# Performance work log

Measured on AMD Instinct MI355X. Metric: run time of the kernel, lower is better.

The kernel has to match this reference:

```python
import jax, jax.numpy as jnp
import numpy as np
import math

N_HEAD = 16
ROPE_BASE = 10000.0


def _rope_as_in_source(x):
    """Faithful replication of RotaryPositionalEmbeddings.forward applied to
    x of shape [B, H, T, hd] (called after transpose in the source, so
    seq_len = x.size(1) = H: angles are indexed by head index, not position)."""
    B, H, T, hd = x.shape
    theta = 1.0 / (ROPE_BASE ** (jnp.arange(0, hd, 2, dtype=jnp.float32) / hd))  # [hd/2]
    ang = jnp.arange(H, dtype=jnp.float32)[:, None] * theta[None, :]  # [H, hd/2]
    cos = jnp.cos(ang)[None, :, None, :]  # [1, H, 1, hd/2]
    sin = jnp.sin(ang)[None, :, None, :]
    xr = x.reshape(B, H, T, hd // 2, 2)
    out = jnp.stack([
        xr[..., 0] * cos - xr[..., 1] * sin,
        xr[..., 1] * cos + xr[..., 0] * sin,
    ], axis=-1)
    return out.reshape(B, H, T, hd)


def setup_inputs() -> dict:
    key = jax.random.key(0)
    ks = jax.random.split(key, 5)
    B, T, C = 2, 2048, 1024
    s = 0.02
    return {
        "x": jax.random.normal(ks[0], (B, T, C), dtype=jnp.float32),
        "W_attn": jax.random.normal(ks[1], (C, 3 * C), dtype=jnp.float32) * s,
        "b_attn": jnp.zeros((3 * C,), dtype=jnp.float32),
        "W_proj": jax.random.normal(ks[2], (C, C), dtype=jnp.float32) * s,
        "b_proj": jnp.zeros((C,), dtype=jnp.float32),
    }


def reference(x, W_attn, b_attn, W_proj, b_proj):
    B, T, C = x.shape
    H = N_HEAD
    hd = C // H
    qkv = x @ W_attn + b_attn  # [B, T, 3C]
    q, k, v = jnp.split(qkv, 3, axis=2)
    # [B, T, H, hd] -> [B, H, T, hd]
    q = q.reshape(B, T, H, hd).transpose(0, 2, 1, 3)
    k = k.reshape(B, T, H, hd).transpose(0, 2, 1, 3)
    v = v.reshape(B, T, H, hd).transpose(0, 2, 1, 3)
    q = _rope_as_in_source(q)
    k = _rope_as_in_source(k)
    att = jnp.einsum("bhqd,bhkd->bhqk", q, k) * (1.0 / math.sqrt(hd))
    causal = jnp.tril(jnp.ones((T, T), dtype=bool))
    att = jnp.where(causal[None, None, :, :], att, -jnp.inf)
    att = jax.nn.softmax(att, axis=-1)
    y = jnp.einsum("bhqk,bhkd->bhqd", att, v)  # [B, H, T, hd]
    y = y.transpose(0, 2, 1, 3).reshape(B, T, C)
    return y @ W_proj + b_proj
```

## Files before the change

### kernel.cpp

```cpp
#include <hip/hip_runtime.h>

typedef __attribute__((ext_vector_type(8))) short bf16x8;
typedef __attribute__((ext_vector_type(4))) float f32x4;
typedef __attribute__((ext_vector_type(4))) unsigned int uint4v;
typedef unsigned short ushort_t;

#define BB 2
#define TT 2048
#define CC 1024
#define HH 16
#define HD 64
#define MM (BB * TT)
#define N3C (3 * CC)
#define KD 1024
#define NT64 16

__device__ __forceinline__ ushort_t f2b(float f) {
  unsigned u = __builtin_bit_cast(unsigned, f);
  u += 0x7fffu + ((u >> 16) & 1u);
  return (ushort_t)(u >> 16);
}

__device__ __forceinline__ unsigned pack2rne(float a, float b) {
  return (unsigned)f2b(a) | ((unsigned)f2b(b) << 16);
}

__device__ __forceinline__ unsigned pack2bf(float a, float b) {
  unsigned ua = (__builtin_bit_cast(unsigned, a) + 0x8000u) >> 16;
  unsigned ub = (__builtin_bit_cast(unsigned, b) + 0x8000u) & 0xffff0000u;
  return ua | ub;
}

__device__ __forceinline__ float fexp2(float x) {
#if __has_builtin(__builtin_amdgcn_exp2f)
  return __builtin_amdgcn_exp2f(x);
#else
  return __expf(x * 0.6931471805599453f);
#endif
}

__device__ __forceinline__ f32x4 mfma16(bf16x8 a, bf16x8 b, f32x4 c) {
  return __builtin_amdgcn_mfma_f32_16x16x32_bf16(a, b, c, 0, 0, 0);
}

__device__ __forceinline__ void load_lds16(const void* g, void* l) {
  __builtin_amdgcn_global_load_lds((const __attribute__((address_space(1))) void*)g,
                                   (__attribute__((address_space(3))) void*)l, 16, 0, 0);
}

#define BAR()   __builtin_amdgcn_s_barrier()
#define SB0()   __builtin_amdgcn_sched_barrier(0)
#define LGKM0() asm volatile("s_waitcnt lgkmcnt(0)" ::: "memory")

__global__ __launch_bounds__(256) void prep(const float* __restrict__ x,
                                            const float* __restrict__ Wa,
                                            const float* __restrict__ Wp,
                                            ushort_t* __restrict__ xb,
                                            ushort_t* __restrict__ wat,
                                            ushort_t* __restrict__ wpt) {
  const int blk = blockIdx.x, tid = threadIdx.x;
  if (blk < 4096) {
    int i = blk * 256 + tid;
    const float4 v = ((const float4*)x)[i];
    typedef __attribute__((ext_vector_type(4))) ushort_t us4;
    us4 r;
    r.x = f2b(v.x); r.y = f2b(v.y); r.z = f2b(v.z); r.w = f2b(v.w);
    ((us4*)xb)[i] = r;
    return;
  }
  __shared__ ushort_t tile[32][33];
  const float* W; ushort_t* Wt; int R, Nc, n0, r0;
  if (blk < 7168) {
    int tb = blk - 4096;
    W = Wa; Wt = wat; R = CC; Nc = N3C;
    n0 = (tb % 96) * 32; r0 = (tb / 96) * 32;
  } else {
    int tb = blk - 7168;
    W = Wp; Wt = wpt; R = CC; Nc = CC;
    n0 = (tb & 31) * 32; r0 = (tb >> 5) * 32;
  }
  const int c = tid & 31, rr = tid >> 5;
#pragma unroll
  for (int i = 0; i < 4; ++i) {
    int r = rr + i * 8;
    tile[r][c] = f2b(W[(size_t)(r0 + r) * Nc + n0 + c]);
  }
  __syncthreads();
#pragma unroll
  for (int i = 0; i < 4; ++i) {
    int r = rr + i * 8;
    Wt[(size_t)(n0 + r) * R + r0 + c] = tile[c][r];
  }
}

__global__ __launch_bounds__(512, 2) void qkv256(const ushort_t* __restrict__ A,
                                                 const ushort_t* __restrict__ Bt,
                                                 const float* __restrict__ bias,
                                                 ushort_t* __restrict__ qo,
                                                 ushort_t* __restrict__ ko,
                                                 ushort_t* __restrict__ vto) {
  extern __shared__ ushort_t lds[];
  ushort_t* As = lds;
  ushort_t* Bs = lds + 32768;

  const int tid = threadIdx.x, lane = tid & 63, wave = tid >> 6;
  const int l15 = lane & 15, quad = lane >> 4;
  const int wm = (wave >> 2) * 128, wn = (wave & 3) * 64;
  const int m0 = blockIdx.y * 256, n0 = blockIdx.x * 256;

  const int rw0 = tid >> 2, gc0 = (tid & 3) ^ (rw0 & 3);
  const ushort_t* sA0 = A + (size_t)(m0 + rw0) * KD + gc0 * 8;
  const ushort_t* sA1 = sA0 + (size_t)128 * KD;
  const ushort_t* sB0 = Bt + (size_t)(n0 + rw0) * KD + gc0 * 8;
  const ushort_t* sB1 = sB0 + (size_t)128 * KD;
  ushort_t* dA0 = As + tid * 8;
  ushort_t* dA1 = dA0 + 4096;
  ushort_t* dB0 = Bs + tid * 8;
  ushort_t* dB1 = dB0 + 4096;

  auto stA = [&](int tau, int kh) {
    const int so = ((tau & 1) * 2 + kh) * 8192;
    const int ko2 = tau * 64 + kh * 32;
    load_lds16(sA0 + ko2, dA0 + so);
    load_lds16(sA1 + ko2, dA1 + so);
  };
  auto stB = [&](int tau, int kh) {
    const int so = ((tau & 1) * 2 + kh) * 8192;
    const int ko2 = tau * 64 + kh * 32;
    load_lds16(sB0 + ko2, dB0 + so);
    load_lds16(sB1 + ko2, dB1 + so);
  };

  const int swc = (quad ^ (l15 & 3)) * 8;
  const int rdA = (wm + l15) * 32 + swc;
  const int rdB = (wn + l15) * 32 + swc;

  f32x4 acc[8][4] = {};

  stB(0, 0); stA(0, 0); stB(0, 1); stA(0, 1);
  stB(1, 0); stA(1, 0); stB(1, 1);
  asm volatile("s_waitcnt vmcnt(6)" ::: "memory");
  BAR();
  SB0();

  bf16x8 a[4], b0[4], b1[4];
  for (int t = 0; t < NT64; ++t) {
    const int par = t & 1;
    const ushort_t* aK0 = As + par * 16384;
    const ushort_t* aK1 = aK0 + 8192;
    const ushort_t* bK0 = Bs + par * 16384;
    const ushort_t* bK1 = bK0 + 8192;

#pragma unroll
    for (int j = 0; j < 4; ++j) b0[j] = *(const bf16x8*)&bK0[rdB + j * 512];
#pragma unroll
    for (int i = 0; i < 4; ++i) a[i] = *(const bf16x8*)&aK0[rdA + i * 512];
    if (t + 1 < NT64) stA(t + 1, 1);
    BAR();
    LGKM0();
    __builtin_amdgcn_s_setprio(1);
#pragma unroll
    for (int i = 0; i < 4; ++i)
#pragma unroll
      for (int j = 0; j < 4; ++j) acc[i][j] = mfma16(a[i], b0[j], acc[i][j]);
    __builtin_amdgcn_s_setprio(0);
    BAR();
    SB0();

#pragma unroll
    for (int i = 0; i < 4; ++i) a[i] = *(const bf16x8*)&aK0[rdA + (4 + i) * 512];
    if (t + 2 < NT64) stB(t + 2, 0);
    BAR();
    LGKM0();
    __builtin_amdgcn_s_setprio(1);
#pragma unroll
    for (int i = 0; i < 4; ++i)
#pragma unroll
      for (int j = 0; j < 4; ++j) acc[4 + i][j] = mfma16(a[i], b0[j], acc[4 + i][j]);
    __builtin_amdgcn_s_setprio(0);
    BAR();
    SB0();

#pragma unroll
    for (int j = 0; j < 4; ++j) b1[j] = *(const bf16x8*)&bK1[rdB + j * 512];
#pragma unroll
    for (int i = 0; i < 4; ++i) a[i] = *(const bf16x8*)&aK1[rdA + i * 512];
    if (t + 2 < NT64) stA(t + 2, 0);
    BAR();
    LGKM0();
    __builtin_amdgcn_s_setprio(1);
#pragma unroll
    for (int i = 0; i < 4; ++i)
#pragma unroll
      for (int j = 0; j < 4; ++j) acc[i][j] = mfma16(a[i], b1[j], acc[i][j]);
    __builtin_amdgcn_s_setprio(0);
    BAR();
    SB0();

#pragma unroll
    for (int i = 0; i < 4; ++i) a[i] = *(const bf16x8*)&aK1[rdA + (4 + i) * 512];
    if (t + 2 < NT64) stB(t + 2, 1);
    if (t < NT64 - 2)       { asm volatile("s_waitcnt vmcnt(6)" ::: "memory"); }
    else if (t == NT64 - 2) { asm volatile("s_waitcnt vmcnt(0)" ::: "memory"); }
    BAR();
    LGKM0();
    __builtin_amdgcn_s_setprio(1);
#pragma unroll
    for (int i = 0; i < 4; ++i)
#pragma unroll
      for (int j = 0; j < 4; ++j) acc[4 + i][j] = mfma16(a[i], b1[j], acc[4 + i][j]);
    __builtin_amdgcn_s_setprio(0);
    BAR();
    SB0();
  }

  float bv[4];
#pragma unroll
  for (int j = 0; j < 4; ++j) bv[j] = bias[n0 + wn + j * 16 + l15];

  const int h8 = l15 >> 3, j8l = l15 & 7;
  const int t0 = (m0 + wm) & 2047, b = (m0 + wm) >> 11;
  const int gsec = (n0 + wn) >> 10, h = ((n0 + wn) & 1023) >> 6;
  const int bh = b * HH + h;
  if (gsec < 2) {
    ushort_t* dst = (gsec == 0 ? qo + ((size_t)bh * 128 + (t0 >> 4)) * 1024
                               : ko + ((size_t)bh * 32 + (t0 >> 6)) * 4096)
                    + h8 * 128 + quad * 32 + j8l;
#pragma unroll
    for (int i = 0; i < 8; ++i)
#pragma unroll
      for (int j = 0; j < 4; ++j)
#pragma unroll
        for (int r = 0; r < 4; ++r)
          dst[i * 1024 + (j >> 1) * 512 + (j & 1) * 256 + r * 8] =
              f2b(acc[i][j][r] + bv[j]);
  } else {
    ushort_t* dst = vto + ((size_t)bh * 32 + (t0 >> 6)) * 4096 + quad * 128 + l15 * 8;
#pragma unroll
    for (int j = 0; j < 4; ++j)
#pragma unroll
      for (int i = 0; i < 8; ++i) {
        uint2 u;
        u.x = pack2rne(acc[i][j][0] + bv[j], acc[i][j][1] + bv[j]);
        u.y = pack2rne(acc[i][j][2] + bv[j], acc[i][j][3] + bv[j]);
        const int il = i & 3;
        *(uint2*)&dst[(i >> 2) * 4096 + j * 1024 + (il >> 1) * 512 + (il & 1) * 4] = u;
      }
  }
}

template <int EPI, int NT>
__global__ __launch_bounds__(256) void gemm_bt(const ushort_t* __restrict__ A,
                                               const ushort_t* __restrict__ Bt,
                                               const float* __restrict__ bias,
                                               ushort_t* __restrict__ qo,
                                               ushort_t* __restrict__ ko,
                                               ushort_t* __restrict__ vto,
                                               float* __restrict__ outp,
                                               int N, int K) {
  constexpr int NJ = NT / 32;
  __shared__ __align__(16) ushort_t As[128 * 64];
  __shared__ __align__(16) ushort_t Bs[NT * 64];
  const int tid = threadIdx.x, lane = tid & 63, wave = tid >> 6;
  const int l15 = lane & 15, quad = lane >> 4;
  const int wm = (wave >> 1) * 64, wn = (wave & 1) * (NT / 2);
  const int m0 = blockIdx.y * 128, n0 = blockIdx.x * NT;

  f32x4 acc[4][NJ] = {};
  for (int k0 = 0; k0 < K; k0 += 64) {
    __syncthreads();
#pragma unroll
    for (int p = 0; p < 4; ++p) {
      int d16 = p * 256 + tid;
      int pan = d16 >> 9, rem = d16 & 511, row = rem >> 2, cc = rem & 3;
      load_lds16(&A[(size_t)(m0 + row) * K + k0 + pan * 32 + cc * 8], &As[d16 * 8]);
    }
#pragma unroll
    for (int p = 0; p < NT / 32; ++p) {
      int d16 = p * 256 + tid;
      int pan = d16 / (NT * 4), rem = d16 % (NT * 4), row = rem >> 2, cc = rem & 3;
      load_lds16(&Bt[(size_t)(n0 + row) * K + k0 + pan * 32 + cc * 8], &Bs[d16 * 8]);
    }
    __syncthreads();
#pragma unroll
    for (int pan = 0; pan < 2; ++pan) {
      const ushort_t* Ap = &As[pan * 4096];
      const ushort_t* Bp = &Bs[pan * (NT * 32)];
      bf16x8 af[4], bfr[NJ];
#pragma unroll
      for (int i = 0; i < 4; ++i)
        af[i] = *(const bf16x8*)&Ap[(wm + i * 16 + l15) * 32 + quad * 8];
#pragma unroll
      for (int j = 0; j < NJ; ++j)
        bfr[j] = *(const bf16x8*)&Bp[(wn + j * 16 + l15) * 32 + quad * 8];
#pragma unroll
      for (int i = 0; i < 4; ++i)
#pragma unroll
        for (int j = 0; j < NJ; ++j)
          acc[i][j] = mfma16(af[i], bfr[j], acc[i][j]);
    }
  }

  float bv[NJ];
#pragma unroll
  for (int j = 0; j < NJ; ++j) bv[j] = bias[n0 + wn + j * 16 + l15];

  if (EPI == 1) {
#pragma unroll
    for (int i = 0; i < 4; ++i)
#pragma unroll
      for (int r = 0; r < 4; ++r) {
        float* rp = outp + (size_t)(m0 + wm + i * 16 + quad * 4 + r) * N + n0 + wn + l15;
#pragma unroll
        for (int j = 0; j < NJ; ++j) rp[j * 16] = acc[i][j][r] + bv[j];
      }
  }
}

__global__ __launch_bounds__(256) void attn_kernel(const ushort_t* __restrict__ Qf,
                                                   const ushort_t* __restrict__ Kf,
                                                   const ushort_t* __restrict__ Vf,
                                                   ushort_t* __restrict__ y) {
  __shared__ __align__(16) float red[2][2176];
  const int tid = threadIdx.x, lane = tid & 63, wave = tid >> 6;
  const int l15 = lane & 15, quad = lane >> 4;
  const int idx = blockIdx.x;
  const int xcd = idx & 7, j = idx >> 3;
  const int bh = xcd * 4 + (j & 3);
  const int g = 63 - (j >> 2);
  const int qs = g * 32;
  const int nk = (qs + 95) >> 6;

  const float SCL = 0.125f * 1.4426950408889634f;

  const ushort_t* qbase = Qf + (((size_t)bh * 128 + (qs >> 4)) * 2 * 64 + lane) * 8;
  bf16x8 qf[2][2];
#pragma unroll
  for (int st = 0; st < 2; ++st)
#pragma unroll
    for (int dh = 0; dh < 2; ++dh)
      qf[st][dh] = *(const bf16x8*)(qbase + (st * 2 + dh) * 512);

  f32x4 o[2][4] = {};
  float l_r[2] = {0.f, 0.f};

  for (int it = wave; it < nk; it += 4) {
    const bool diag = (it == nk - 1);
    const size_t tb = ((size_t)bh * 32 + it) * 4096 + (size_t)lane * 8;
    bf16x8 kf[4][2], vf[4][2];
#pragma unroll
    for (int ng = 0; ng < 4; ++ng)
#pragma unroll
      for (int dh = 0; dh < 2; ++dh)
        kf[ng][dh] = *(const bf16x8*)(Kf + tb + (ng * 2 + dh) * 512);
#pragma unroll
    for (int dg = 0; dg < 4; ++dg)
#pragma unroll
      for (int h = 0; h < 2; ++h)
        vf[dg][h] = *(const bf16x8*)(Vf + tb + (dg * 2 + h) * 512);

#pragma unroll
    for (int st = 0; st < 2; ++st) {
      f32x4 s[4];
#pragma unroll
      for (int ng = 0; ng < 4; ++ng) {
        f32x4 z = {};
        z = mfma16(kf[ng][0], qf[st][0], z);
        z = mfma16(kf[ng][1], qf[st][1], z);
        s[ng] = z;
      }
      float p[4][4];
      const int qg = qs + st * 16 + l15;
#pragma unroll
      for (int ng = 0; ng < 4; ++ng)
#pragma unroll
        for (int r = 0; r < 4; ++r) {
          float pv = fexp2(s[ng][r] * SCL);
          if (diag) {
            int kg = it * 64 + ng * 16 + quad * 4 + r;
            pv = (kg > qg) ? 0.f : pv;
          }
          p[ng][r] = pv;
          l_r[st] += pv;
        }
      union { uint4v u; bf16x8 v; } pk0, pk1;
      pk0.u[0] = pack2bf(p[0][0], p[0][1]); pk0.u[1] = pack2bf(p[0][2], p[0][3]);
      pk0.u[2] = pack2bf(p[1][0], p[1][1]); pk0.u[3] = pack2bf(p[1][2], p[1][3]);
      pk1.u[0] = pack2bf(p[2][0], p[2][1]); pk1.u[1] = pack2bf(p[2][2], p[2][3]);
      pk1.u[2] = pack2bf(p[3][0], p[3][1]); pk1.u[3] = pack2bf(p[3][2], p[3][3]);
#pragma unroll
      for (int dg = 0; dg < 4; ++dg) {
        o[st][dg] = mfma16(vf[dg][0], pk0.v, o[st][dg]);
        o[st][dg] = mfma16(vf[dg][1], pk1.v, o[st][dg]);
      }
    }
  }

  auto dump = [&](float* buf) {
#pragma unroll
    for (int st = 0; st < 2; ++st)
#pragma unroll
      for (int dg = 0; dg < 4; ++dg)
        *(f32x4*)&buf[(st * 4 + dg) * 256 + lane * 4] = o[st][dg];
    buf[2048 + lane * 2 + 0] = l_r[0];
    buf[2048 + lane * 2 + 1] = l_r[1];
  };
  auto merge = [&](const float* buf) {
#pragma unroll
    for (int st = 0; st < 2; ++st)
#pragma unroll
      for (int dg = 0; dg < 4; ++dg)
        o[st][dg] += *(const f32x4*)&buf[(st * 4 + dg) * 256 + lane * 4];
    l_r[0] += buf[2048 + lane * 2 + 0];
    l_r[1] += buf[2048 + lane * 2 + 1];
  };
  if (wave == 1) dump(red[0]);
  if (wave == 3) dump(red[1]);
  __syncthreads();
  if (wave == 0) merge(red[0]);
  if (wave == 2) merge(red[1]);
  __syncthreads();
  if (wave == 2) dump(red[0]);
  __syncthreads();
  if (wave == 0) {
    merge(red[0]);
    const int b = bh >> 4, h = bh & 15;
#pragma unroll
    for (int st = 0; st < 2; ++st) {
      float lf = l_r[st];
      lf += __shfl_xor(lf, 16);
      lf += __shfl_xor(lf, 32);
      const float inv = 1.0f / lf;
      const size_t row = (size_t)(b * TT + qs + st * 16 + l15) * CC;
#pragma unroll
      for (int dg = 0; dg < 4; ++dg) {
        uint2 u;
        u.x = pack2rne(o[st][dg][0] * inv, o[st][dg][1] * inv);
        u.y = pack2rne(o[st][dg][2] * inv, o[st][dg][3] * inv);
        *(uint2*)&y[row + h * HD + dg * 16 + quad * 4] = u;
      }
    }
  }
}

extern "C" void kernel_launch(void* const* d_in, const int* in_sizes, int n_in,
                              void* d_out, int out_size, void* d_ws, size_t ws_size,
                              hipStream_t stream) {
  const float* x  = (const float*)d_in[0];
  const float* Wa = (const float*)d_in[1];
  const float* ba = (const float*)d_in[2];
  const float* Wp = (const float*)d_in[3];
  const float* bp = (const float*)d_in[4];
  float* out = (float*)d_out;

  char* ws = (char*)d_ws;
  ushort_t* xb  = (ushort_t*)(ws + 0);
  ushort_t* wat = (ushort_t*)(ws + 8388608);
  ushort_t* wpt = (ushort_t*)(ws + 14680064);
  ushort_t* Qf  = (ushort_t*)(ws + 16777216);
  ushort_t* Kf  = (ushort_t*)(ws + 25165824);
  ushort_t* Vf  = (ushort_t*)(ws + 33554432);
  ushort_t* yb  = (ushort_t*)(ws + 41943040);

  static int attr_done = 0;
  if (!attr_done) {
    (void)hipFuncSetAttribute((const void*)qkv256,
                              hipFuncAttributeMaxDynamicSharedMemorySize, 131072);
    attr_done = 1;
  }

  prep<<<8192, 256, 0, stream>>>(x, Wa, Wp, xb, wat, wpt);

  qkv256<<<dim3(N3C / 256, MM / 256), 512, 131072, stream>>>(xb, wat, ba, Qf, Kf, Vf);

  attn_kernel<<<2048, 256, 0, stream>>>(Qf, Kf, Vf, yb);

  gemm_bt<1, 64><<<dim3(CC / 64, MM / 128), 256, 0, stream>>>(
      yb, wpt, bp, nullptr, nullptr, nullptr, out, CC, CC);
}
```

Measured before the change: 175.9 us.

## Remap QKV GEMM blocks per XCD, change LDS swizzle, use inline ds_read offsets

Remaps the linear block id so that blocks sharing A/B tiles land on the same XCD, aiming for better L2 reuse across the 16x12 grid. Changes the LDS XOR swizzle to use (row>>1)&3, intended to reduce bank conflicts for the 16-row MFMA reads. Replaces the compiler-generated LDS reads with inline-asm ds_read_b128 using immediate offsets, which cuts address arithmetic. Adds sched barriers after the waitcnts. The grid remap hardcodes the 12x16 shape and assumes round-robin block-to-XCD dispatch.

```diff
diff --git a/kernel.cpp b/kernel.cpp
--- a/kernel.cpp
+++ b/kernel.cpp
@@ -51,6 +51,17 @@
 #define BAR()   __builtin_amdgcn_s_barrier()
 #define SB0()   __builtin_amdgcn_sched_barrier(0)
 #define LGKM0() asm volatile("s_waitcnt lgkmcnt(0)" ::: "memory")
+
+using lds_p = const __attribute__((address_space(3))) ushort_t*;
+template <int OFF>
+__device__ __forceinline__ bf16x8 dsr128o(lds_p a) {
+  bf16x8 r;
+  asm volatile("ds_read_b128 %0, %1 offset:%2" : "=v"(r) : "v"(a), "i"(OFF));
+  return r;
+}
+#define RD4(dst, base, off0)                                                   \
+  dst[0] = dsr128o<(off0)>(base);        dst[1] = dsr128o<(off0) + 1024>(base);\
+  dst[2] = dsr128o<(off0) + 2048>(base); dst[3] = dsr128o<(off0) + 3072>(base);
 
 __global__ __launch_bounds__(256) void prep(const float* __restrict__ x,
                                             const float* __restrict__ Wa,
@@ -106,9 +117,14 @@
   const int tid = threadIdx.x, lane = tid & 63, wave = tid >> 6;
   const int l15 = lane & 15, quad = lane >> 4;
   const int wm = (wave >> 2) * 128, wn = (wave & 3) * 64;
-  const int m0 = blockIdx.y * 256, n0 = blockIdx.x * 256;
-
-  const int rw0 = tid >> 2, gc0 = (tid & 3) ^ (rw0 & 3);
+
+  const int bid = blockIdx.y * 12 + blockIdx.x;
+  const int xcd = bid & 7, idx = bid >> 3;
+  const int by = (xcd >> 1) * 4 + idx / 6;
+  const int bx = (xcd & 1) * 6 + idx % 6;
+  const int m0 = by * 256, n0 = bx * 256;
+
+  const int rw0 = tid >> 2, gc0 = (tid & 3) ^ ((rw0 >> 1) & 3);
   const ushort_t* sA0 = A + (size_t)(m0 + rw0) * KD + gc0 * 8;
   const ushort_t* sA1 = sA0 + (size_t)128 * KD;
   const ushort_t* sB0 = Bt + (size_t)(n0 + rw0) * KD + gc0 * 8;
@@ -131,9 +147,11 @@
     load_lds16(sB1 + ko2, dB1 + so);
   };
 
-  const int swc = (quad ^ (l15 & 3)) * 8;
+  const int swc = (quad ^ ((l15 >> 1) & 3)) * 8;
   const int rdA = (wm + l15) * 32 + swc;
   const int rdB = (wn + l15) * 32 + swc;
+  lds_p A3 = (lds_p)As;
+  lds_p B3 = (lds_p)Bs;
 
   f32x4 acc[8][4] = {};
 
@@ -146,18 +164,15 @@
   bf16x8 a[4], b0[4], b1[4];
   for (int t = 0; t < NT64; ++t) {
     const int par = t & 1;
-    const ushort_t* aK0 = As + par * 16384;
-    const ushort_t* aK1 = aK0 + 8192;
-    const ushort_t* bK0 = Bs + par * 16384;
-    const ushort_t* bK1 = bK0 + 8192;
-
-#pragma unroll
-    for (int j = 0; j < 4; ++j) b0[j] = *(const bf16x8*)&bK0[rdB + j * 512];
-#pragma unroll
-    for (int i = 0; i < 4; ++i) a[i] = *(const bf16x8*)&aK0[rdA + i * 512];
+    lds_p pA = A3 + par * 16384 + rdA;
+    lds_p pB = B3 + par * 16384 + rdB;
+
+    RD4(b0, pB, 0);
+    RD4(a, pA, 0);
     if (t + 1 < NT64) stA(t + 1, 1);
     BAR();
     LGKM0();
+    SB0();
     __builtin_amdgcn_s_setprio(1);
 #pragma unroll
     for (int i = 0; i < 4; ++i)
@@ -167,11 +182,11 @@
     BAR();
     SB0();
 
-#pragma unroll
-    for (int i = 0; i < 4; ++i) a[i] = *(const bf16x8*)&aK0[rdA + (4 + i) * 512];
+    RD4(a, pA, 4096);
     if (t + 2 < NT64) stB(t + 2, 0);
     BAR();
     LGKM0();
+    SB0();
     __builtin_amdgcn_s_setprio(1);
 #pragma unroll
     for (int i = 0; i < 4; ++i)
@@ -181,13 +196,12 @@
     BAR();
     SB0();
 
-#pragma unroll
-    for (int j = 0; j < 4; ++j) b1[j] = *(const bf16x8*)&bK1[rdB + j * 512];
-#pragma unroll
-    for (int i = 0; i < 4; ++i) a[i] = *(const bf16x8*)&aK1[rdA + i * 512];
+    RD4(b1, pB, 16384);
+    RD4(a, pA, 16384);
     if (t + 2 < NT64) stA(t + 2, 0);
     BAR();
     LGKM0();
+    SB0();
     __builtin_amdgcn_s_setprio(1);
 #pragma unroll
     for (int i = 0; i < 4; ++i)
@@ -197,13 +211,13 @@
     BAR();
     SB0();
 
-#pragma unroll
-    for (int i = 0; i < 4; ++i) a[i] = *(const bf16x8*)&aK1[rdA + (4 + i) * 512];
+    RD4(a, pA, 16384 + 4096);
     if (t + 2 < NT64) stB(t + 2, 1);
     if (t < NT64 - 2)       { asm volatile("s_waitcnt vmcnt(6)" ::: "memory"); }
     else if (t == NT64 - 2) { asm volatile("s_waitcnt vmcnt(0)" ::: "memory"); }
     BAR();
     LGKM0();
+    SB0();
     __builtin_amdgcn_s_setprio(1);
 #pragma unroll
     for (int i = 0; i < 4; ++i)
```

Result: no change. 172.8 us (-1.8%).
